# Optimization experiments

Measured on AMD Instinct MI355X. Metric: run time of the kernel, lower is better.

Reference implementation:

```python
import jax, jax.numpy as jnp
import numpy as np

EPS = 1e-6
WEIGHT_THRESHOLD = 0.0


def setup_inputs() -> dict:
    key = jax.random.key(0)
    kA, kB, kW = jax.random.split(key, 3)
    bs, n = 200000, 20
    A = jax.random.normal(kA, (bs, n, 3), dtype=jnp.float32)
    B = jax.random.normal(kB, (bs, n, 3), dtype=jnp.float32)
    weights = jax.random.uniform(kW, (bs, n), dtype=jnp.float32)
    return {"A": A, "B": B, "weights": weights}


def reference(A, B, weights):
    """Batched weighted Procrustes (Kabsch). A,B: [bs,n,3], weights: [bs,n].
    Returns SE3 transforms [bs,4,4], matching rigid_transform_3d + integrate_trans."""
    w = jnp.where(weights < WEIGHT_THRESHOLD, 0.0, weights)
    wsum = jnp.sum(w, axis=1, keepdims=True)[:, :, None] + EPS  # [bs,1,1]
    centroid_A = jnp.sum(A * w[:, :, None], axis=1, keepdims=True) / wsum  # [bs,1,3]
    centroid_B = jnp.sum(B * w[:, :, None], axis=1, keepdims=True) / wsum
    Am = A - centroid_A
    Bm = B - centroid_B
    # H = Am^T diag(w) Bm  -> [bs,3,3]
    H = jnp.einsum('bni,bn,bnj->bij', Am, w, Bm)
    U, S, Vh = jnp.linalg.svd(H)          # H = U S Vh
    V = jnp.swapaxes(Vh, -1, -2)          # torch.svd's "Vt" is actually V
    Ut = jnp.swapaxes(U, -1, -2)
    delta = jnp.linalg.det(V @ Ut)        # [bs]
    corr = jnp.broadcast_to(jnp.eye(3, dtype=A.dtype), V.shape).copy()
    corr = corr.at[:, 2, 2].set(delta)
    R = V @ corr @ Ut                     # [bs,3,3]
    t = jnp.swapaxes(centroid_B, 1, 2) - R @ jnp.swapaxes(centroid_A, 1, 2)  # [bs,3,1]
    top = jnp.concatenate([R, t], axis=-1)  # [bs,3,4]
    bottom = jnp.broadcast_to(jnp.array([0.0, 0.0, 0.0, 1.0], dtype=A.dtype), (A.shape[0], 1, 4))
    return jnp.concatenate([top, bottom], axis=1)  # [bs,4,4]
```

## Files before the change

### kernel.cpp

```cpp
#include <hip/hip_runtime.h>

#define EPS_W 1e-6f
#define IPB 128

__device__ __forceinline__ float fast_rsq(float x) { return __builtin_amdgcn_rsqf(x); }
__device__ __forceinline__ float fast_rcp(float x) { return __builtin_amdgcn_rcpf(x); }

__device__ __forceinline__ void solve16(const float S[16], float R[9], float t[3])
{
    const float sw  = S[0];
    const float Sa0 = S[1], Sa1 = S[2], Sa2 = S[3];
    const float Sb0 = S[4], Sb1 = S[5], Sb2 = S[6];

    const float inv = fast_rcp(sw + EPS_W);
    const float cA0 = Sa0*inv, cA1 = Sa1*inv, cA2 = Sa2*inv;
    const float cB0 = Sb0*inv, cB1 = Sb1*inv, cB2 = Sb2*inv;

    float H[3][3];
    H[0][0] = S[7]  - cA0*Sb0 - Sa0*cB0 + sw*cA0*cB0;
    H[0][1] = S[8]  - cA0*Sb1 - Sa0*cB1 + sw*cA0*cB1;
    H[0][2] = S[9]  - cA0*Sb2 - Sa0*cB2 + sw*cA0*cB2;
    H[1][0] = S[10] - cA1*Sb0 - Sa1*cB0 + sw*cA1*cB0;
    H[1][1] = S[11] - cA1*Sb1 - Sa1*cB1 + sw*cA1*cB1;
    H[1][2] = S[12] - cA1*Sb2 - Sa1*cB2 + sw*cA1*cB2;
    H[2][0] = S[13] - cA2*Sb0 - Sa2*cB0 + sw*cA2*cB0;
    H[2][1] = S[14] - cA2*Sb1 - Sa2*cB1 + sw*cA2*cB1;
    H[2][2] = S[15] - cA2*Sb2 - Sa2*cB2 + sw*cA2*cB2;

    const float Sxx=H[0][0], Sxy=H[0][1], Sxz=H[0][2];
    const float Syx=H[1][0], Syy=H[1][1], Syz=H[1][2];
    const float Szx=H[2][0], Szy=H[2][1], Szz=H[2][2];

    float Nm[4][4];
    Nm[0][0] =  Sxx+Syy+Szz; Nm[0][1] = Syz-Szy;      Nm[0][2] = Szx-Sxz;      Nm[0][3] = Sxy-Syx;
    Nm[1][0] =  Nm[0][1];    Nm[1][1] = Sxx-Syy-Szz;  Nm[1][2] = Sxy+Syx;      Nm[1][3] = Szx+Sxz;
    Nm[2][0] =  Nm[0][2];    Nm[2][1] = Nm[1][2];     Nm[2][2] = -Sxx+Syy-Szz; Nm[2][3] = Syz+Szy;
    Nm[3][0] =  Nm[0][3];    Nm[3][1] = Nm[1][3];     Nm[3][2] = Nm[2][3];     Nm[3][3] = -Sxx-Syy+Szz;

    float Vv[4][4] = {{1.f,0.f,0.f,0.f},{0.f,1.f,0.f,0.f},{0.f,0.f,1.f,0.f},{0.f,0.f,0.f,1.f}};

    for (int sweep = 0; sweep < 5; ++sweep) {
        #pragma unroll
        for (int pair = 0; pair < 6; ++pair) {
            constexpr int PP[6] = {0,0,0,1,1,2};
            constexpr int QQ[6] = {1,2,3,2,3,3};
            const int p = PP[pair], q = QQ[pair];
            float d  = Nm[p][p] - Nm[q][q];
            float o  = Nm[p][q];
            float r2 = d*d + 4.f*o*o;
            bool tiny = r2 < 1e-30f;
            float rinv = fast_rsq(tiny ? 1.f : r2);
            float hh = 0.5f + 0.5f * fabsf(d) * rinv;
            float ci = fast_rsq(hh);
            float c  = hh * ci;
            float s  = (d < 0.f ? o : -o) * rinv * ci;
            c = tiny ? 1.f : c;
            s = tiny ? 0.f : s;
            #pragma unroll
            for (int k = 0; k < 4; ++k) {
                float akp = Nm[k][p], akq = Nm[k][q];
                Nm[k][p] = c*akp - s*akq;
                Nm[k][q] = s*akp + c*akq;
            }
            #pragma unroll
            for (int k = 0; k < 4; ++k) {
                float apk = Nm[p][k], aqk = Nm[q][k];
                Nm[p][k] = c*apk - s*aqk;
                Nm[q][k] = s*apk + c*aqk;
            }
            #pragma unroll
            for (int k = 0; k < 4; ++k) {
                float vkp = Vv[k][p], vkq = Vv[k][q];
                Vv[k][p] = c*vkp - s*vkq;
                Vv[k][q] = s*vkp + c*vkq;
            }
        }
    }

    float q0=Vv[0][0], q1=Vv[1][0], q2=Vv[2][0], q3=Vv[3][0];
    float best = Nm[0][0];
    #pragma unroll
    for (int m = 1; m < 4; ++m) {
        bool bt = Nm[m][m] > best;
        best = bt ? Nm[m][m] : best;
        q0 = bt ? Vv[0][m] : q0;
        q1 = bt ? Vv[1][m] : q1;
        q2 = bt ? Vv[2][m] : q2;
        q3 = bt ? Vv[3][m] : q3;
    }
    float qn = fast_rsq(q0*q0 + q1*q1 + q2*q2 + q3*q3);
    q0*=qn; q1*=qn; q2*=qn; q3*=qn;

    float R00 = q0*q0+q1*q1-q2*q2-q3*q3;
    float R01 = 2.f*(q1*q2 - q0*q3);
    float R02 = 2.f*(q1*q3 + q0*q2);
    float R10 = 2.f*(q1*q2 + q0*q3);
    float R11 = q0*q0-q1*q1+q2*q2-q3*q3;
    float R12 = 2.f*(q2*q3 - q0*q1);
    float R20 = 2.f*(q1*q3 - q0*q2);
    float R21 = 2.f*(q2*q3 + q0*q1);
    float R22 = q0*q0-q1*q1-q2*q2+q3*q3;

    float trRH  = R00*Sxx+R01*Syx+R02*Szx
                + R10*Sxy+R11*Syy+R12*Szy
                + R20*Sxz+R21*Syz+R22*Szz;
    float trRtH = R00*Sxx+R01*Sxy+R02*Sxz
                + R10*Syx+R11*Syy+R12*Syz
                + R20*Szx+R21*Szy+R22*Szz;
    if (trRtH > trRH) {
        float tt;
        tt = R01; R01 = R10; R10 = tt;
        tt = R02; R02 = R20; R20 = tt;
        tt = R12; R12 = R21; R21 = tt;
    }

    R[0]=R00; R[1]=R01; R[2]=R02;
    R[3]=R10; R[4]=R11; R[5]=R12;
    R[6]=R20; R[7]=R21; R[8]=R22;
    t[0] = cB0 - (R00*cA0 + R01*cA1 + R02*cA2);
    t[1] = cB1 - (R10*cA0 + R11*cA1 + R12*cA2);
    t[2] = cB2 - (R20*cA0 + R21*cA1 + R22*cA2);
}

__global__ __launch_bounds__(256, 4) void kabsch_swz20_kernel(
    const float* __restrict__ A, const float* __restrict__ B,
    const float* __restrict__ W, float* __restrict__ Out, int bs)
{
    __shared__ float sbuf[8192];
    float4* s4 = reinterpret_cast<float4*>(sbuf);
    float2* s2 = reinterpret_cast<float2*>(sbuf);

    const int tid  = threadIdx.x;
    const int base = blockIdx.x * IPB;
    int itemcnt = bs - base;
    if (itemcnt > IPB) itemcnt = IPB;

    const int i = tid >> 1;
    const int h = tid & 1;
    const bool act = (i < itemcnt);

    const float4* Wg = reinterpret_cast<const float4*>(W) + (size_t)base * 5;
    const int nW4 = itemcnt * 5;
    for (int g = tid; g < nW4; g += 256) {
        const int it = g / 5, c = g - it * 5;
        s4[it * 6 + c] = Wg[g];
    }
    __syncthreads();
    float wv[10];
    if (act) {
        #pragma unroll
        for (int g = 0; g < 5; ++g) {
            float2 v = s2[i * 12 + 5 * h + g];
            wv[2*g] = v.x; wv[2*g+1] = v.y;
        }
    }
    __syncthreads();

    const float4* Ag = reinterpret_cast<const float4*>(A) + (size_t)base * 15;
    const int n4 = itemcnt * 15;
    for (int g = tid; g < n4; g += 256) {
        const int it = g / 15, c = g - it * 15;
        s4[(it << 4) + (c ^ (it & 15))] = Ag[g];
    }
    __syncthreads();
    float2 av[15];
    if (act) {
        #pragma unroll
        for (int j = 0; j < 15; ++j) {
            const int s = 15 * h + j;
            const int c = s >> 1, r = s & 1;
            av[j] = s2[(i << 5) + (((c ^ (i & 15)) << 1) | r)];
        }
    }
    __syncthreads();

    const float4* Bg = reinterpret_cast<const float4*>(B) + (size_t)base * 15;
    for (int g = tid; g < n4; g += 256) {
        const int it = g / 15, c = g - it * 15;
        s4[(it << 4) + (c ^ (it & 15))] = Bg[g];
    }
    __syncthreads();
    float2 bv[15];
    if (act) {
        #pragma unroll
        for (int j = 0; j < 15; ++j) {
            const int s = 15 * h + j;
            const int c = s >> 1, r = s & 1;
            bv[j] = s2[(i << 5) + (((c ^ (i & 15)) << 1) | r)];
        }
    }

    float S[16];
    #pragma unroll
    for (int k = 0; k < 16; ++k) S[k] = 0.f;
    if (act) {
        #pragma unroll
        for (int g = 0; g < 5; ++g) {
            float2 a0 = av[3*g+0], a1 = av[3*g+1], a2 = av[3*g+2];
            float2 b0 = bv[3*g+0], b1 = bv[3*g+1], b2 = bv[3*g+2];
            float w0 = wv[2*g]   < 0.f ? 0.f : wv[2*g];
            float w1 = wv[2*g+1] < 0.f ? 0.f : wv[2*g+1];
            {
                float ax=a0.x, ay=a0.y, az=a1.x;
                float bx=b0.x, by=b0.y, bz=b1.x;
                S[0] += w0;
                float wax=w0*ax, way=w0*ay, waz=w0*az;
                S[1]+=wax; S[2]+=way; S[3]+=waz;
                S[4]+=w0*bx; S[5]+=w0*by; S[6]+=w0*bz;
                S[7] +=wax*bx; S[8] +=wax*by; S[9] +=wax*bz;
                S[10]+=way*bx; S[11]+=way*by; S[12]+=way*bz;
                S[13]+=waz*bx; S[14]+=waz*by; S[15]+=waz*bz;
            }
            {
                float ax=a1.y, ay=a2.x, az=a2.y;
                float bx=b1.y, by=b2.x, bz=b2.y;
                S[0] += w1;
                float wax=w1*ax, way=w1*ay, waz=w1*az;
                S[1]+=wax; S[2]+=way; S[3]+=waz;
                S[4]+=w1*bx; S[5]+=w1*by; S[6]+=w1*bz;
                S[7] +=wax*bx; S[8] +=wax*by; S[9] +=wax*bz;
                S[10]+=way*bx; S[11]+=way*by; S[12]+=way*bz;
                S[13]+=waz*bx; S[14]+=waz*by; S[15]+=waz*bz;
            }
        }
    }

    #pragma unroll
    for (int k = 0; k < 16; ++k) S[k] += __shfl_xor(S[k], 1);

    __syncthreads();
    if (h == 0 && act) {
        #pragma unroll
        for (int k = 0; k < 16; ++k) sbuf[17 * i + k] = S[k];
    }
    __syncthreads();

    if (tid < itemcnt) {
        float Ss[16];
        #pragma unroll
        for (int k = 0; k < 16; ++k) Ss[k] = sbuf[17 * tid + k];
        float R[9], t[3];
        solve16(Ss, R, t);
        float4* O4 = reinterpret_cast<float4*>(Out + (size_t)(base + tid) * 16);
        O4[0] = make_float4(R[0], R[1], R[2], t[0]);
        O4[1] = make_float4(R[3], R[4], R[5], t[1]);
        O4[2] = make_float4(R[6], R[7], R[8], t[2]);
        O4[3] = make_float4(0.f, 0.f, 0.f, 1.f);
    }
}

__global__ __launch_bounds__(256) void kabsch_generic_kernel(
    const float* __restrict__ A, const float* __restrict__ B,
    const float* __restrict__ W, float* __restrict__ Out,
    int bs, int n)
{
    const int b = blockIdx.x * blockDim.x + threadIdx.x;
    if (b >= bs) return;

    float S[16];
    #pragma unroll
    for (int k = 0; k < 16; ++k) S[k] = 0.f;

    for (int j = 0; j < n; ++j) {
        const float* ap = A + ((size_t)b * n + j) * 3;
        const float* bp = B + ((size_t)b * n + j) * 3;
        float w = W[(size_t)b * n + j];
        w = w < 0.f ? 0.f : w;
        float ax=ap[0], ay=ap[1], az=ap[2];
        float bx=bp[0], by=bp[1], bz=bp[2];
        S[0] += w;
        float wax = w*ax, way = w*ay, waz = w*az;
        S[1] += wax; S[2] += way; S[3] += waz;
        S[4] += w*bx; S[5] += w*by; S[6] += w*bz;
        S[7] += wax*bx; S[8]  += wax*by; S[9]  += wax*bz;
        S[10]+= way*bx; S[11] += way*by; S[12] += way*bz;
        S[13]+= waz*bx; S[14] += waz*by; S[15] += waz*bz;
    }

    float R[9], t[3];
    solve16(S, R, t);

    float4* O4 = reinterpret_cast<float4*>(Out + (size_t)b * 16);
    O4[0] = make_float4(R[0], R[1], R[2], t[0]);
    O4[1] = make_float4(R[3], R[4], R[5], t[1]);
    O4[2] = make_float4(R[6], R[7], R[8], t[2]);
    O4[3] = make_float4(0.f, 0.f, 0.f, 1.f);
}

extern "C" void kernel_launch(void* const* d_in, const int* in_sizes, int n_in,
                              void* d_out, int out_size, void* d_ws, size_t ws_size,
                              hipStream_t stream) {
    const float* A = (const float*)d_in[0];
    const float* B = (const float*)d_in[1];
    const float* W = (const float*)d_in[2];
    float* Out = (float*)d_out;
    const int bs = out_size / 16;
    const int n  = (bs > 0) ? (in_sizes[2] / bs) : 0;
    if (n == 20) {
        const int blocks = (bs + IPB - 1) / IPB;
        hipLaunchKernelGGL(kabsch_swz20_kernel, dim3(blocks), dim3(256), 0, stream,
                           A, B, W, Out, bs);
    } else {
        const int blocks = (bs + 255) / 256;
        hipLaunchKernelGGL(kabsch_generic_kernel, dim3(blocks), dim3(256), 0, stream,
                           A, B, W, Out, bs, n);
    }
}
```

Measured before the change: 166.9 us.

## Replace LDS-staged block kernel with single-wave kernel loading directly from global

New measurement: 150.1 us. 10.1% less time.

```diff
diff --git a/kernel.cpp b/kernel.cpp
--- a/kernel.cpp
+++ b/kernel.cpp
@@ -1,7 +1,6 @@
 #include <hip/hip_runtime.h>
 
 #define EPS_W 1e-6f
-#define IPB 128
 
 __device__ __forceinline__ float fast_rsq(float x) { return __builtin_amdgcn_rsqf(x); }
 __device__ __forceinline__ float fast_rcp(float x) { return __builtin_amdgcn_rcpf(x); }
@@ -122,84 +121,46 @@
     t[2] = cB2 - (R20*cA0 + R21*cA1 + R22*cA2);
 }
 
-__global__ __launch_bounds__(256, 4) void kabsch_swz20_kernel(
+__global__ __launch_bounds__(64, 4) void kabsch_wave20_kernel(
     const float* __restrict__ A, const float* __restrict__ B,
     const float* __restrict__ W, float* __restrict__ Out, int bs)
 {
-    __shared__ float sbuf[8192];
-    float4* s4 = reinterpret_cast<float4*>(sbuf);
-    float2* s2 = reinterpret_cast<float2*>(sbuf);
-
-    const int tid  = threadIdx.x;
-    const int base = blockIdx.x * IPB;
-    int itemcnt = bs - base;
-    if (itemcnt > IPB) itemcnt = IPB;
-
-    const int i = tid >> 1;
-    const int h = tid & 1;
-    const bool act = (i < itemcnt);
-
-    const float4* Wg = reinterpret_cast<const float4*>(W) + (size_t)base * 5;
-    const int nW4 = itemcnt * 5;
-    for (int g = tid; g < nW4; g += 256) {
-        const int it = g / 5, c = g - it * 5;
-        s4[it * 6 + c] = Wg[g];
-    }
-    __syncthreads();
-    float wv[10];
-    if (act) {
-        #pragma unroll
-        for (int g = 0; g < 5; ++g) {
-            float2 v = s2[i * 12 + 5 * h + g];
-            wv[2*g] = v.x; wv[2*g+1] = v.y;
-        }
-    }
-    __syncthreads();
-
-    const float4* Ag = reinterpret_cast<const float4*>(A) + (size_t)base * 15;
-    const int n4 = itemcnt * 15;
-    for (int g = tid; g < n4; g += 256) {
-        const int it = g / 15, c = g - it * 15;
-        s4[(it << 4) + (c ^ (it & 15))] = Ag[g];
-    }
-    __syncthreads();
-    float2 av[15];
-    if (act) {
-        #pragma unroll
-        for (int j = 0; j < 15; ++j) {
-            const int s = 15 * h + j;
-            const int c = s >> 1, r = s & 1;
-            av[j] = s2[(i << 5) + (((c ^ (i & 15)) << 1) | r)];
-        }
-    }
-    __syncthreads();
-
-    const float4* Bg = reinterpret_cast<const float4*>(B) + (size_t)base * 15;
-    for (int g = tid; g < n4; g += 256) {
-        const int it = g / 15, c = g - it * 15;
-        s4[(it << 4) + (c ^ (it & 15))] = Bg[g];
-    }
-    __syncthreads();
-    float2 bv[15];
-    if (act) {
-        #pragma unroll
-        for (int j = 0; j < 15; ++j) {
-            const int s = 15 * h + j;
-            const int c = s >> 1, r = s & 1;
-            bv[j] = s2[(i << 5) + (((c ^ (i & 15)) << 1) | r)];
-        }
-    }
-
-    float S[16];
-    #pragma unroll
-    for (int k = 0; k < 16; ++k) S[k] = 0.f;
-    if (act) {
+    __shared__ float sums[64 * 17];
+
+    const int lane = threadIdx.x;
+    const int base = blockIdx.x * 64;
+    const int i = lane >> 1;
+    const int h = lane & 1;
+
+    const float2* A2 = reinterpret_cast<const float2*>(A);
+    const float2* B2 = reinterpret_cast<const float2*>(B);
+    const float2* W2 = reinterpret_cast<const float2*>(W);
+
+    #pragma unroll
+    for (int grp = 0; grp < 2; ++grp) {
+        int item  = base + grp * 32 + i;
+        int itemc = item < bs ? item : bs - 1;
+        const int abase = itemc * 30 + h * 15;
+        const int wbase = itemc * 10 + h * 5;
+
+        float2 av[15], bv[15], wv2[5];
+        #pragma unroll
+        for (int j = 0; j < 15; ++j) av[j] = A2[abase + j];
+        #pragma unroll
+        for (int j = 0; j < 15; ++j) bv[j] = B2[abase + j];
+        #pragma unroll
+        for (int j = 0; j < 5;  ++j) wv2[j] = W2[wbase + j];
+
+        float S[16];
+        #pragma unroll
+        for (int k = 0; k < 16; ++k) S[k] = 0.f;
+
         #pragma unroll
         for (int g = 0; g < 5; ++g) {
             float2 a0 = av[3*g+0], a1 = av[3*g+1], a2 = av[3*g+2];
             float2 b0 = bv[3*g+0], b1 = bv[3*g+1], b2 = bv[3*g+2];
-            float w0 = wv[2*g]   < 0.f ? 0.f : wv[2*g];
-            float w1 = wv[2*g+1] < 0.f ? 0.f : wv[2*g+1];
+            float w0 = wv2[g].x < 0.f ? 0.f : wv2[g].x;
+            float w1 = wv2[g].y < 0.f ? 0.f : wv2[g].y;
             {
                 float ax=a0.x, ay=a0.y, az=a1.x;
                 float bx=b0.x, by=b0.y, bz=b1.x;
@@ -223,29 +184,41 @@
                 S[13]+=waz*bx; S[14]+=waz*by; S[15]+=waz*bz;
             }
         }
-    }
-
-    #pragma unroll
-    for (int k = 0; k < 16; ++k) S[k] += __shfl_xor(S[k], 1);
-
-    __syncthreads();
-    if (h == 0 && act) {
-        #pragma unroll
-        for (int k = 0; k < 16; ++k) sbuf[17 * i + k] = S[k];
-    }
-    __syncthreads();
-
-    if (tid < itemcnt) {
-        float Ss[16];
-        #pragma unroll
-        for (int k = 0; k < 16; ++k) Ss[k] = sbuf[17 * tid + k];
-        float R[9], t[3];
-        solve16(Ss, R, t);
-        float4* O4 = reinterpret_cast<float4*>(Out + (size_t)(base + tid) * 16);
-        O4[0] = make_float4(R[0], R[1], R[2], t[0]);
-        O4[1] = make_float4(R[3], R[4], R[5], t[1]);
-        O4[2] = make_float4(R[6], R[7], R[8], t[2]);
-        O4[3] = make_float4(0.f, 0.f, 0.f, 1.f);
+
+        #pragma unroll
+        for (int k = 0; k < 16; ++k) S[k] += __shfl_xor(S[k], 1);
+
+        if (h == 0) {
+            const int row = grp * 32 + i;
+            #pragma unroll
+            for (int k = 0; k < 16; ++k) sums[row * 17 + k] = S[k];
+        }
+    }
+
+    float Ss[16];
+    #pragma unroll
+    for (int k = 0; k < 16; ++k) Ss[k] = sums[lane * 17 + k];
+
+    float R[9], t[3];
+    solve16(Ss, R, t);
+
+    {
+        float* o = &sums[lane * 17];
+        o[0]=R[0];  o[1]=R[1];  o[2]=R[2];  o[3]=t[0];
+        o[4]=R[3];  o[5]=R[4];  o[6]=R[5];  o[7]=t[1];
+        o[8]=R[6];  o[9]=R[7];  o[10]=R[8]; o[11]=t[2];
+        o[12]=0.f;  o[13]=0.f;  o[14]=0.f;  o[15]=1.f;
+    }
+
+    float4* Og = reinterpret_cast<float4*>(Out) + (size_t)base * 4;
+    #pragma unroll
+    for (int j2 = 0; j2 < 4; ++j2) {
+        const int j  = j2 * 64 + lane;
+        const int it = j >> 2;
+        if (base + it < bs) {
+            const float* o = &sums[it * 17 + (j & 3) * 4];
+            Og[j] = make_float4(o[0], o[1], o[2], o[3]);
+        }
     }
 }
 
@@ -297,8 +270,8 @@
     const int bs = out_size / 16;
     const int n  = (bs > 0) ? (in_sizes[2] / bs) : 0;
     if (n == 20) {
-        const int blocks = (bs + IPB - 1) / IPB;
-        hipLaunchKernelGGL(kabsch_swz20_kernel, dim3(blocks), dim3(256), 0, stream,
+        const int blocks = (bs + 63) / 64;
+        hipLaunchKernelGGL(kabsch_wave20_kernel, dim3(blocks), dim3(64), 0, stream,
                            A, B, W, Out, bs);
     } else {
         const int blocks = (bs + 255) / 256;
```
